# Optimization experiments

Hardware: AMD Instinct MI355X
Metric: run time of the kernel (lower is better)

The kernel has to match this reference:

```python
import jax, jax.numpy as jnp
import numpy as np
from functools import partial

GAMMA = 1.0
LAM = 1.0
N_ITER = 60  # fixed iteration count for the projected-gradient dual fused-lasso solver
GROUP_TOL = 1e-6


def _gfl_solve_row(x, A, lam):
    """Graph fused lasso: argmin_y 0.5||y-x||^2 + lam*sum_ij A_ij |y_i - y_j|.
    Solved by projected gradient ascent on the dual (edge flows z_ij in [-lam*A_ij, lam*A_ij]).
    x: [N], A: [N, N] -> y: [N]
    """
    N = x.shape[0]
    w = lam * A
    step = jnp.asarray(1.0 / (2.0 * N), dtype=x.dtype)

    def body(z, _):
        y = x - jnp.sum(z, axis=1) + jnp.sum(z, axis=0)  # primal from flows
        z = jnp.clip(z + step * (y[:, None] - y[None, :]), -w, w)
        return z, None

    z, _ = jax.lax.scan(body, jnp.zeros_like(A), None, length=N_ITER)
    return x - jnp.sum(z, axis=1) + jnp.sum(z, axis=0)


@partial(jax.custom_vjp, nondiff_argnums=(2,))
def gfusedlasso(x, A, lam):
    # x: [B, N], A: [B, N, N]
    return jax.vmap(_gfl_solve_row, in_axes=(0, 0, None))(x, A, lam)


def _gfl_fwd(x, A, lam):
    out = gfusedlasso(x, A, lam)
    return out, out


def _gfl_bwd(lam, out, g):
    # Faithful to backward_gfusedmax_torch_1D: average grad over groups of equal outputs.
    eq = (jnp.abs(out[:, :, None] - out[:, None, :]) < GROUP_TOL).astype(g.dtype)  # [B,N,N]
    grad_x = jnp.einsum('bij,bj->bi', eq, g) / jnp.sum(eq, axis=2)
    return grad_x, jnp.zeros_like(eq)  # no gradient defined for A (matches torch)


gfusedlasso.defvjp(_gfl_fwd, _gfl_bwd)


def sparsemax(x, axis=-1):
    # torch_sparsemax.forward with gamma=1.0
    N = x.shape[axis]
    x_sorted = jnp.flip(jnp.sort(x, axis=axis), axis=axis)  # descending
    cumsum = jnp.cumsum(x_sorted, axis=axis)
    k = jnp.arange(1, N + 1, dtype=x.dtype)  # broadcast along last axis
    mask = (1.0 + k * x_sorted > cumsum).astype(x.dtype)
    tau = (jnp.sum(x_sorted * mask, axis=axis, keepdims=True) - 1.0) / jnp.sum(mask, axis=axis, keepdims=True)
    return jnp.maximum(x - tau, 0.0)


def setup_inputs() -> dict:
    key = jax.random.key(0)
    kx, ka = jax.random.split(key)
    B, N = 4096, 128
    x = jax.random.normal(kx, (B, N), dtype=jnp.float32)
    A = jax.random.uniform(ka, (B, N, N), dtype=jnp.float32)
    return {"x": x, "A": A}


def reference(x, A):
    # Gfusedmax.forward: x/gamma -> gfusedlasso(lam/gamma) -> sparsemax(gamma=1)
    xg = x / GAMMA
    fused = gfusedlasso(xg, A, LAM / GAMMA)
    return sparsemax(fused, axis=-1)
```

## Files before the change

### kernel.cpp

```cpp
#include <hip/hip_runtime.h>

#define N 128
#define NITER 60
#define PST 132
#define COLOFF 2128
#define GBUF (COLOFF + 16 * PST)

typedef float v2f __attribute__((ext_vector_type(2)));
typedef float v4f __attribute__((ext_vector_type(4)));

__global__ __launch_bounds__(512, 2)
void gfusedmax_kernel(const float* __restrict__ x,
                      const float* __restrict__ A,
                      float* __restrict__ out)
{
    const int tid = threadIdx.x;
    const int grp = tid >> 8;
    const int lt  = tid & 255;
    const int tr  = lt >> 4;
    const int tc  = lt & 15;
    const int i0  = tr * 8;
    const int j0  = tc * 8;
    const int row = blockIdx.x * 2 + grp;

    __shared__ __align__(16) float parts[2][GBUF];
    __shared__ __align__(16) float yv[2][N];
    __shared__ float sorted[2][N];
    __shared__ float red[2][8];

    const float step = 1.0f / 256.0f;

    v2f w2[8][4];
    v2f z2[8][4];
    const float* Ab = A + (size_t)row * N * N;
    #pragma unroll
    for (int r = 0; r < 8; ++r) {
        const v4f* src = (const v4f*)(Ab + (size_t)(i0 + r) * N + j0);
        v4f p0 = src[0];
        v4f p1 = src[1];
        w2[r][0] = p0.lo; w2[r][1] = p0.hi;
        w2[r][2] = p1.lo; w2[r][3] = p1.hi;
        #pragma unroll
        for (int cp = 0; cp < 4; ++cp) z2[r][cp] = (v2f)0.0f;
    }

    const int m = lt >> 1;
    const float xm = x[(size_t)row * N + m];
    const float* pb = &parts[grp][0] + ((lt & 1) ? COLOFF : 0);
    float* yvg = yv[grp];

    if (lt < N) yvg[lt] = step * x[(size_t)row * N + lt];
    __syncthreads();

    auto UPDATE = [&]() {
        v2f drs[8], ec2[4];
        #pragma unroll
        for (int r = 0; r < 8; ++r) drs[r] = (v2f)yvg[i0 + r];
        v4f e0 = *(const v4f*)&yvg[j0];
        v4f e1 = *(const v4f*)&yvg[j0 + 4];
        ec2[0] = e0.lo; ec2[1] = e0.hi;
        ec2[2] = e1.lo; ec2[3] = e1.hi;
        v2f pr2[8], pc2[4];
        #pragma unroll
        for (int r = 0; r < 8; ++r) {
            #pragma unroll
            for (int cp = 0; cp < 4; ++cp) {
                v2f t  = (z2[r][cp] + drs[r]) - ec2[cp];
                v2f wv = w2[r][cp];
                v2f zn;
                zn.x = __builtin_amdgcn_fmed3f(t.x, -wv.x, wv.x);
                zn.y = __builtin_amdgcn_fmed3f(t.y, -wv.y, wv.y);
                z2[r][cp] = zn;
                pr2[r]  = (cp == 0) ? zn : pr2[r] + zn;
                pc2[cp] = (r == 0)  ? zn : pc2[cp] + zn;
            }
        }
        v4f r0, r1, c0, c1;
        r0.x = pr2[0].x + pr2[0].y;  r0.y = pr2[1].x + pr2[1].y;
        r0.z = pr2[2].x + pr2[2].y;  r0.w = pr2[3].x + pr2[3].y;
        r1.x = pr2[4].x + pr2[4].y;  r1.y = pr2[5].x + pr2[5].y;
        r1.z = pr2[6].x + pr2[6].y;  r1.w = pr2[7].x + pr2[7].y;
        c0.x = pc2[0].x; c0.y = pc2[0].y; c0.z = pc2[1].x; c0.w = pc2[1].y;
        c1.x = pc2[2].x; c1.y = pc2[2].y; c1.z = pc2[3].x; c1.w = pc2[3].y;
        *(v4f*)&parts[grp][tc * PST + i0]              = r0;
        *(v4f*)&parts[grp][tc * PST + i0 + 4]          = r1;
        *(v4f*)&parts[grp][COLOFF + tr * PST + j0]     = c0;
        *(v4f*)&parts[grp][COLOFF + tr * PST + j0 + 4] = c1;
    };

    auto REDUCE = [&](bool raw) {
        float acc = 0.0f;
        #pragma unroll
        for (int k = 0; k < 16; ++k) acc += pb[k * PST + m];
        float other = __shfl_xor(acc, 1, 64);
        if (!(lt & 1)) {
            float y = (xm - acc) + other;
            yvg[m] = raw ? y : step * y;
        }
    };

    for (int t = 0; t <= NITER; ++t) {
        if (grp == 0) { if (t < NITER) UPDATE(); }
        else          { if (t > 0) REDUCE(t == NITER); }
        __syncthreads();
        if (t == NITER) break;
        if (grp == 1) UPDATE();
        else          REDUCE(t == NITER - 1);
        __syncthreads();
    }

    float* sog = sorted[grp];
    float v = 0.0f;
    if (lt < N) {
        v = yvg[lt];
        int rk = 0;
        for (int k = 0; k < N; ++k) {
            float u = yvg[k];
            rk += (u > v) || (u == v && k < lt);
        }
        sog[rk] = v;
    }
    __syncthreads();

    float s = 0.0f, csum = 0.0f;
    if (lt < N) {
        s = sog[lt];
        for (int mm = 0; mm < N; ++mm) {
            float u = sog[mm];
            if (mm <= lt) csum += u;
        }
    }
    bool maskb = (lt < N) && (1.0f + (float)(lt + 1) * s > csum);
    float aRed = maskb ? s : 0.0f;
    float bRed = maskb ? 1.0f : 0.0f;
    #pragma unroll
    for (int off = 32; off >= 1; off >>= 1) {
        aRed += __shfl_down(aRed, off, 64);
        bRed += __shfl_down(bRed, off, 64);
    }
    const int wid = lt >> 6;
    if ((lt & 63) == 0) { red[grp][wid * 2] = aRed; red[grp][wid * 2 + 1] = bRed; }
    __syncthreads();
    const float tau = (red[grp][0] + red[grp][2] + red[grp][4] + red[grp][6] - 1.0f)
                    / (red[grp][1] + red[grp][3] + red[grp][5] + red[grp][7]);
    if (lt < N) out[(size_t)row * N + lt] = fmaxf(v - tau, 0.0f);
}

extern "C" void kernel_launch(void* const* d_in, const int* in_sizes, int n_in,
                              void* d_out, int out_size, void* d_ws, size_t ws_size,
                              hipStream_t stream) {
    const float* x = (const float*)d_in[0];
    const float* A = (const float*)d_in[1];
    float* out = (float*)d_out;
    const int B = in_sizes[0] / N;
    gfusedmax_kernel<<<B / 2, 512, 0, stream>>>(x, A, out);
}
```

Baseline: 1.012 ms.

## Split both rows across all threads and interleave update with reduction

```diff
diff --git a/kernel.cpp b/kernel.cpp
--- a/kernel.cpp
+++ b/kernel.cpp
@@ -2,26 +2,82 @@
 
 #define N 128
 #define NITER 60
-#define PST 132
-#define COLOFF 2128
-#define GBUF (COLOFF + 16 * PST)
+#define RPS 132
+#define COLB (32 * RPS + 16)
+#define GBUF (COLB + 16 * RPS)
 
 typedef float v2f __attribute__((ext_vector_type(2)));
 typedef float v4f __attribute__((ext_vector_type(4)));
+
+template<int Q, int P>
+__device__ __forceinline__ void window_step(
+    v2f (&z2)[2][8][2], const v2f (&w2)[2][8][2],
+    float (&parts)[2][GBUF], float (&yv)[2][N],
+    const float* pbP, int q, int m,
+    int tr, int tc, int i0, int j0,
+    float xmP, bool doUpd, bool store, bool raw)
+{
+    const float step = 1.0f / 256.0f;
+
+    float rt[16];
+    #pragma unroll
+    for (int k = 0; k < 16; ++k) rt[k] = pbP[k * RPS];
+
+    if (doUpd) {
+        float* yq = yv[Q];
+        v4f ev = *(const v4f*)&yq[j0];
+        v2f ec0 = ev.lo, ec1 = ev.hi;
+        float rowp[8];
+        v2f pc0, pc1;
+        #pragma unroll
+        for (int r = 0; r < 8; ++r) {
+            v2f dr = (v2f)yq[i0 + r];
+            v2f t0 = (z2[Q][r][0] + dr) - ec0;
+            v2f t1 = (z2[Q][r][1] + dr) - ec1;
+            v2f wv0 = w2[Q][r][0], wv1 = w2[Q][r][1];
+            v2f zn0, zn1;
+            zn0.x = __builtin_amdgcn_fmed3f(t0.x, -wv0.x, wv0.x);
+            zn0.y = __builtin_amdgcn_fmed3f(t0.y, -wv0.y, wv0.y);
+            zn1.x = __builtin_amdgcn_fmed3f(t1.x, -wv1.x, wv1.x);
+            zn1.y = __builtin_amdgcn_fmed3f(t1.y, -wv1.y, wv1.y);
+            z2[Q][r][0] = zn0;
+            z2[Q][r][1] = zn1;
+            v2f pr = zn0 + zn1;
+            rowp[r] = pr.x + pr.y;
+            pc0 = (r == 0) ? zn0 : pc0 + zn0;
+            pc1 = (r == 0) ? zn1 : pc1 + zn1;
+        }
+        v4f r0v, r1v, c0v;
+        r0v.x = rowp[0]; r0v.y = rowp[1]; r0v.z = rowp[2]; r0v.w = rowp[3];
+        r1v.x = rowp[4]; r1v.y = rowp[5]; r1v.z = rowp[6]; r1v.w = rowp[7];
+        c0v.x = pc0.x; c0v.y = pc0.y; c0v.z = pc1.x; c0v.w = pc1.y;
+        *(v4f*)&parts[Q][tc * RPS + i0]        = r0v;
+        *(v4f*)&parts[Q][tc * RPS + i0 + 4]    = r1v;
+        *(v4f*)&parts[Q][COLB + tr * RPS + j0] = c0v;
+    }
+
+    float acc = 0.0f;
+    #pragma unroll
+    for (int k = 0; k < 16; ++k) acc += rt[k];
+    float acc2  = acc + __shfl_xor(acc, 1, 64);
+    float other = __shfl_xor(acc2, 2, 64);
+    if (store && q == 0) {
+        float y = (xmP - acc2) + 0.5f * other;
+        yv[P][m] = raw ? y : step * y;
+    }
+}
 
 __global__ __launch_bounds__(512, 2)
 void gfusedmax_kernel(const float* __restrict__ x,
                       const float* __restrict__ A,
                       float* __restrict__ out)
 {
+    const int b0  = blockIdx.x * 2;
     const int tid = threadIdx.x;
-    const int grp = tid >> 8;
-    const int lt  = tid & 255;
-    const int tr  = lt >> 4;
-    const int tc  = lt & 15;
+    const int tr  = tid >> 5;
+    const int tc  = tid & 31;
     const int i0  = tr * 8;
-    const int j0  = tc * 8;
-    const int row = blockIdx.x * 2 + grp;
+    const int j0  = tc * 4;
 
     __shared__ __align__(16) float parts[2][GBUF];
     __shared__ __align__(16) float yv[2][N];
@@ -30,85 +86,45 @@
 
     const float step = 1.0f / 256.0f;
 
-    v2f w2[8][4];
-    v2f z2[8][4];
-    const float* Ab = A + (size_t)row * N * N;
+    v2f w2[2][8][2];
+    v2f z2[2][8][2];
     #pragma unroll
-    for (int r = 0; r < 8; ++r) {
-        const v4f* src = (const v4f*)(Ab + (size_t)(i0 + r) * N + j0);
-        v4f p0 = src[0];
-        v4f p1 = src[1];
-        w2[r][0] = p0.lo; w2[r][1] = p0.hi;
-        w2[r][2] = p1.lo; w2[r][3] = p1.hi;
+    for (int qq = 0; qq < 2; ++qq) {
+        const float* Ab = A + (size_t)(b0 + qq) * N * N;
         #pragma unroll
-        for (int cp = 0; cp < 4; ++cp) z2[r][cp] = (v2f)0.0f;
+        for (int r = 0; r < 8; ++r) {
+            v4f p = *(const v4f*)(Ab + (size_t)(i0 + r) * N + j0);
+            w2[qq][r][0] = p.lo; w2[qq][r][1] = p.hi;
+            z2[qq][r][0] = (v2f)0.0f; z2[qq][r][1] = (v2f)0.0f;
+        }
     }
 
-    const int m = lt >> 1;
-    const float xm = x[(size_t)row * N + m];
-    const float* pb = &parts[grp][0] + ((lt & 1) ? COLOFF : 0);
-    float* yvg = yv[grp];
+    const int m = tid >> 2;
+    const int q = tid & 3;
+    const float xm0 = x[(size_t)b0 * N + m];
+    const float xm1 = x[(size_t)(b0 + 1) * N + m];
+    const float* pb0 = &parts[0][0] + ((q == 0) ? m : (q == 1) ? (16 * RPS + m) : (COLB + m));
+    const float* pb1 = &parts[1][0] + ((q == 0) ? m : (q == 1) ? (16 * RPS + m) : (COLB + m));
 
-    if (lt < N) yvg[lt] = step * x[(size_t)row * N + lt];
+    if (tid < N) {
+        yv[0][tid] = step * x[(size_t)b0 * N + tid];
+        yv[1][tid] = step * x[(size_t)(b0 + 1) * N + tid];
+    }
     __syncthreads();
 
-    auto UPDATE = [&]() {
-        v2f drs[8], ec2[4];
-        #pragma unroll
-        for (int r = 0; r < 8; ++r) drs[r] = (v2f)yvg[i0 + r];
-        v4f e0 = *(const v4f*)&yvg[j0];
-        v4f e1 = *(const v4f*)&yvg[j0 + 4];
-        ec2[0] = e0.lo; ec2[1] = e0.hi;
-        ec2[2] = e1.lo; ec2[3] = e1.hi;
-        v2f pr2[8], pc2[4];
-        #pragma unroll
-        for (int r = 0; r < 8; ++r) {
-            #pragma unroll
-            for (int cp = 0; cp < 4; ++cp) {
-                v2f t  = (z2[r][cp] + drs[r]) - ec2[cp];
-                v2f wv = w2[r][cp];
-                v2f zn;
-                zn.x = __builtin_amdgcn_fmed3f(t.x, -wv.x, wv.x);
-                zn.y = __builtin_amdgcn_fmed3f(t.y, -wv.y, wv.y);
-                z2[r][cp] = zn;
-                pr2[r]  = (cp == 0) ? zn : pr2[r] + zn;
-                pc2[cp] = (r == 0)  ? zn : pc2[cp] + zn;
-            }
-        }
-        v4f r0, r1, c0, c1;
-        r0.x = pr2[0].x + pr2[0].y;  r0.y = pr2[1].x + pr2[1].y;
-        r0.z = pr2[2].x + pr2[2].y;  r0.w = pr2[3].x + pr2[3].y;
-        r1.x = pr2[4].x + pr2[4].y;  r1.y = pr2[5].x + pr2[5].y;
-        r1.z = pr2[6].x + pr2[6].y;  r1.w = pr2[7].x + pr2[7].y;
-        c0.x = pc2[0].x; c0.y = pc2[0].y; c0.z = pc2[1].x; c0.w = pc2[1].y;
-        c1.x = pc2[2].x; c1.y = pc2[2].y; c1.z = pc2[3].x; c1.w = pc2[3].y;
-        *(v4f*)&parts[grp][tc * PST + i0]              = r0;
-        *(v4f*)&parts[grp][tc * PST + i0 + 4]          = r1;
-        *(v4f*)&parts[grp][COLOFF + tr * PST + j0]     = c0;
-        *(v4f*)&parts[grp][COLOFF + tr * PST + j0 + 4] = c1;
-    };
-
-    auto REDUCE = [&](bool raw) {
-        float acc = 0.0f;
-        #pragma unroll
-        for (int k = 0; k < 16; ++k) acc += pb[k * PST + m];
-        float other = __shfl_xor(acc, 1, 64);
-        if (!(lt & 1)) {
-            float y = (xm - acc) + other;
-            yvg[m] = raw ? y : step * y;
-        }
-    };
-
     for (int t = 0; t <= NITER; ++t) {
-        if (grp == 0) { if (t < NITER) UPDATE(); }
-        else          { if (t > 0) REDUCE(t == NITER); }
+        window_step<0, 1>(z2, w2, parts, yv, pb1, q, m, tr, tc, i0, j0,
+                          xm1, t < NITER, t > 0, t == NITER);
         __syncthreads();
         if (t == NITER) break;
-        if (grp == 1) UPDATE();
-        else          REDUCE(t == NITER - 1);
+        window_step<1, 0>(z2, w2, parts, yv, pb0, q, m, tr, tc, i0, j0,
+                          xm0, true, true, t == NITER - 1);
         __syncthreads();
     }
 
+    const int grp = tid >> 8;
+    const int lt  = tid & 255;
+    float* yvg = yv[grp];
     float* sog = sorted[grp];
     float v = 0.0f;
     if (lt < N) {
@@ -143,7 +159,7 @@
     __syncthreads();
     const float tau = (red[grp][0] + red[grp][2] + red[grp][4] + red[grp][6] - 1.0f)
                     / (red[grp][1] + red[grp][3] + red[grp][5] + red[grp][7]);
-    if (lt < N) out[(size_t)row * N + lt] = fmaxf(v - tau, 0.0f);
+    if (lt < N) out[(size_t)(b0 + grp) * N + lt] = fmaxf(v - tau, 0.0f);
 }
 
 extern "C" void kernel_launch(void* const* d_in, const int* in_sizes, int n_in,
```

Measured after the change: 1.109 ms. +9.6%, slower.
